# Kernel tuning notes

Measured on AMD Instinct MI355X. Metric: run time of the kernel, lower is better.

## Reference

```python
import jax, jax.numpy as jnp
import numpy as np

N = 100000
E = 1600000
F_IN = 512
S_IN = 6
H = 64
C = 7


def gcn_conv(x, W, b, row, col, n):
    # PyG GCNConv: linear (no bias in lin), add self-loops, sym-normalize, scatter-add, + bias
    x = x @ W  # [N, out]
    loop = jnp.arange(n)
    r = jnp.concatenate([row, loop])
    c = jnp.concatenate([col, loop])
    deg = jax.ops.segment_sum(jnp.ones(r.shape, x.dtype), c, num_segments=n)
    dinv = jnp.where(deg > 0, deg ** -0.5, 0.0)
    norm = dinv[r] * dinv[c]  # [E+N]
    out = jax.ops.segment_sum(x[r] * norm[:, None], c, num_segments=n)
    return out + b


def setup_inputs() -> dict:
    key = jax.random.key(0)
    ks = jax.random.split(key, 12)
    feature = jax.random.normal(ks[0], (N, F_IN), jnp.float32)
    structure = jax.random.normal(ks[1], (N, S_IN), jnp.float32)
    edge_index = jax.random.randint(ks[2], (2, E), 0, N, dtype=jnp.int64)
    # glorot-ish param init
    def w(k, fan_in, fan_out):
        return jax.random.normal(k, (fan_in, fan_out), jnp.float32) * (1.0 / np.sqrt(fan_in))
    return {
        "feature": feature,
        "structure": structure,
        "edge_index": edge_index,
        "W_f": w(ks[3], F_IN, H), "b_f": jnp.zeros((H,), jnp.float32),
        "W_s": w(ks[4], S_IN, H), "b_s": jnp.zeros((H,), jnp.float32),
        "W_r": w(ks[5], 2 * H, C), "b_r": jnp.zeros((C,), jnp.float32),
        "emb": jax.random.normal(ks[6], (6, H), jnp.float32),
        "embW": jax.random.normal(ks[7], (H, 1), jnp.float32),
        "alpha_s": jnp.asarray(0.4, jnp.float32),
        "alpha_a": jnp.asarray(0.6, jnp.float32),
    }


def reference(feature, structure, edge_index, W_f, b_f, W_s, b_s, W_r, b_r, emb, embW, alpha_s, alpha_a):
    row, col = edge_index[0], edge_index[1]
    # branch 1: feature GCN (dropout is identity in eval mode)
    h_f = gcn_conv(feature, W_f, b_f, row, col, N)
    attr = h_f
    # embedding gate: sigmoid(emb @ embW) thresholded at 0.5 -> {0,1}
    gate = jax.nn.sigmoid(emb @ embW)  # [6,1]
    gate = jnp.where(gate < 0.5, 0.0, 1.0).astype(feature.dtype)
    struct_in = structure * gate[:, 0][None, :]  # [N,6] * [1,6]
    # branch 2: structure GCN
    h_s = gcn_conv(struct_in, W_s, b_s, row, col, N)
    struc = h_s
    # L1-normalize alphas (0.4,0.6 already sum to 1; torch does it via .data)
    denom = jax.lax.stop_gradient(jnp.abs(alpha_s) + jnp.abs(alpha_a))
    a_s = alpha_s / denom
    a_a = alpha_a / denom
    x = jnp.concatenate([attr * a_a * 2.0, struc * a_s * 2.0], axis=1)  # [N, 2H]
    y = gcn_conv(x, W_r, b_r, row, col, N)
    return (h_f, h_s, y)
```

## Files before the change

### kernel.cpp

```cpp
#include <hip/hip_runtime.h>
#include <hip/hip_bf16.h>


typedef __attribute__((ext_vector_type(8))) short bf16x8;
typedef __attribute__((ext_vector_type(4))) float f32x4;

__device__ __forceinline__ unsigned short f2bf(float x) {
    union { __hip_bfloat16 b; unsigned short u; } cv;
    cv.b = __float2bfloat16(x);
    return cv.u;
}
__device__ __forceinline__ float bf2f(unsigned short u) {
    union { unsigned u32; float f; } cv;
    cv.u32 = ((unsigned)u) << 16;
    return cv.f;
}

__global__ __launch_bounds__(256) void setup_prep_k(const float* __restrict__ emb,
                                                    const float* __restrict__ embW,
                                                    const float* __restrict__ alpha_s,
                                                    const float* __restrict__ alpha_a,
                                                    float* __restrict__ cw,
                                                    const float* __restrict__ Wf,
                                                    unsigned short* __restrict__ WthG,
                                                    unsigned short* __restrict__ WtlG,
                                                    unsigned* __restrict__ deg, int n) {
    if (blockIdx.x == 0) {
        if (threadIdx.x >= 64) return;
        int lane = threadIdx.x;
        float w = embW[lane];
        #pragma unroll
        for (int k = 0; k < 6; k++) {
            float p = emb[k * 64 + lane] * w;
            #pragma unroll
            for (int off = 32; off; off >>= 1) p += __shfl_xor(p, off);
            if (lane == 0) cw[k] = (p < 0.0f) ? 0.0f : 1.0f;
        }
        if (lane == 0) {
            float s = alpha_s[0];
            float a = alpha_a[0];
            float inv = 1.0f / (fabsf(s) + fabsf(a));
            cw[6] = 2.0f * a * inv;
            cw[7] = 2.0f * s * inv;
        }
        return;
    }
    if (blockIdx.x <= 128) {
        int idx = (blockIdx.x - 1) * 256 + threadIdx.x;
        int k = idx >> 6, c = idx & 63;
        float w = Wf[idx];
        unsigned short h = f2bf(w);
        unsigned short l = f2bf(w - bf2f(h));
        WthG[c * 512 + k] = h;
        WtlG[c * 512 + k] = l;
        return;
    }
    int start = (blockIdx.x - 129) * 1024 + threadIdx.x;
    #pragma unroll
    for (int k = 0; k < 4; k++) {
        int w = start + k * 256;
        if (w < n) deg[w] = 0u;
    }
}

__device__ __forceinline__ bool detect32(const int* p32, int e, int E, int lane) {
    int se = (e < E) ? e : lane;
    return __any(p32[2 * se + 1] != 0);
}

__global__ void degfill_k(const void* __restrict__ ei, unsigned* __restrict__ deg,
                          int* __restrict__ slot, int E) {
    int e = blockIdx.x * 256 + threadIdx.x;
    int lane = threadIdx.x & 63;
    const int* p32 = (const int*)ei;
    bool is32 = detect32(p32, e, E, lane);
    if (e >= E) return;
    int r, c;
    if (is32) {
        r = p32[e]; c = p32[E + e];
    } else {
        const long long* p = (const long long*)ei;
        r = (int)p[e]; c = (int)p[(size_t)E + e];
    }
    unsigned pos = atomicAdd(&deg[c], 1u);
    if (pos < 64u) slot[((size_t)c << 6) + pos] = r;
}

__global__ void dinv_ss6_k(const unsigned* __restrict__ deg, float* __restrict__ dinv,
                           const float* __restrict__ structure, const float* __restrict__ cw,
                           unsigned short* __restrict__ ss6, int n) {
    int i = blockIdx.x * 256 + threadIdx.x;
    if (i >= n) return;
    float dv = rsqrtf((float)deg[i] + 1.0f);
    dinv[i] = dv;
    #pragma unroll
    for (int k = 0; k < 6; k++) ss6[i * 8 + k] = f2bf(structure[i * 6 + k] * cw[k] * dv);
    ss6[i * 8 + 6] = 0;
    ss6[i * 8 + 7] = 0;
}

__global__ __launch_bounds__(256) void gemm_f_mfma(const float* __restrict__ feat,
                                                   const unsigned short* __restrict__ WthG,
                                                   const unsigned short* __restrict__ WtlG,
                                                   const float* __restrict__ dinv,
                                                   unsigned short* __restrict__ xs, int n) {
    __shared__ unsigned short Ah[128 * 64];
    __shared__ unsigned short Bh[64 * 64];
    __shared__ unsigned short Bl[64 * 64];

    const int tid = threadIdx.x;
    const int blk = blockIdx.x;
    const int w = tid >> 6, l = tid & 63;
    const int lr = l & 15, lg = l >> 4;

    f32x4 acc[2][4];
    #pragma unroll
    for (int m = 0; m < 2; m++)
        #pragma unroll
        for (int nt = 0; nt < 4; nt++) acc[m][nt] = (f32x4)(0.0f);

    const int sr = tid >> 1, shalf = tid & 1;
    const int swc = tid >> 2, swq = tid & 3;
    const int gr_ld = min(blk * 128 + sr, n - 1);
    const float* asrc = feat + (size_t)gr_ld * 512 + shalf * 32;

    for (int k0 = 0; k0 < 512; k0 += 64) {
        {
            const float4* s4 = (const float4*)(asrc + k0);
            int base = sr * 128 + shalf * 64;
            int sw = (sr & 7) << 4;
            #pragma unroll
            for (int g = 0; g < 8; g++) {
                float4 v = s4[g];
                ushort4 h;
                h.x = f2bf(v.x); h.y = f2bf(v.y); h.z = f2bf(v.z); h.w = f2bf(v.w);
                *(ushort4*)((char*)Ah + ((base + g * 8) ^ sw)) = h;
            }
        }
        {
            int sw = (swc & 7) << 4;
            const unsigned short* wh = WthG + swc * 512 + k0;
            const unsigned short* wl = WtlG + swc * 512 + k0;
            #pragma unroll
            for (int s = 0; s < 2; s++) {
                int ko16 = swq * 2 + s;
                uint4 vh = *(const uint4*)(wh + ko16 * 8);
                uint4 vl = *(const uint4*)(wl + ko16 * 8);
                int off = (swc * 128 + ko16 * 16) ^ sw;
                *(uint4*)((char*)Bh + off) = vh;
                *(uint4*)((char*)Bl + off) = vl;
            }
        }
        __syncthreads();
        int swl = (lr & 7) << 4;
        #pragma unroll
        for (int ks = 0; ks < 2; ks++) {
            int koff = ks * 64 + lg * 16;
            int ra = ((w * 32 + lr) * 128 + koff) ^ swl;
            bf16x8 ah0 = *(const bf16x8*)((const char*)Ah + ra);
            bf16x8 ah1 = *(const bf16x8*)((const char*)Ah + ra + 16 * 128);
            #pragma unroll
            for (int nt = 0; nt < 4; nt++) {
                int cb = ((nt * 16 + lr) * 128 + koff) ^ swl;
                bf16x8 bh = *(const bf16x8*)((const char*)Bh + cb);
                bf16x8 bl = *(const bf16x8*)((const char*)Bl + cb);
                acc[0][nt] = __builtin_amdgcn_mfma_f32_16x16x32_bf16(ah0, bh, acc[0][nt], 0, 0, 0);
                acc[0][nt] = __builtin_amdgcn_mfma_f32_16x16x32_bf16(ah0, bl, acc[0][nt], 0, 0, 0);
                acc[1][nt] = __builtin_amdgcn_mfma_f32_16x16x32_bf16(ah1, bh, acc[1][nt], 0, 0, 0);
                acc[1][nt] = __builtin_amdgcn_mfma_f32_16x16x32_bf16(ah1, bl, acc[1][nt], 0, 0, 0);
            }
        }
        __syncthreads();
    }
    #pragma unroll
    for (int m = 0; m < 2; m++) {
        int row0 = blk * 128 + w * 32 + m * 16 + lg * 4;
        #pragma unroll
        for (int reg = 0; reg < 4; reg++) {
            int gr = row0 + reg;
            if (gr < n) {
                float dv = dinv[gr];
                #pragma unroll
                for (int nt = 0; nt < 4; nt++)
                    xs[(size_t)gr * 64 + nt * 16 + lr] = f2bf(acc[m][nt][reg] * dv);
            }
        }
    }
}

#define GATHER8(rl, g, accv, a6v)                                              \
    {                                                                          \
        int r0 = __shfl(rl, g + 0), r1 = __shfl(rl, g + 1);                    \
        int r2 = __shfl(rl, g + 2), r3 = __shfl(rl, g + 3);                    \
        int r4 = __shfl(rl, g + 4), r5 = __shfl(rl, g + 5);                    \
        int r6 = __shfl(rl, g + 6), r7 = __shfl(rl, g + 7);                    \
        float v0 = bf2f(xs[(size_t)r0 * 64 + lane]);                           \
        float v1 = bf2f(xs[(size_t)r1 * 64 + lane]);                           \
        float v2 = bf2f(xs[(size_t)r2 * 64 + lane]);                           \
        float v3 = bf2f(xs[(size_t)r3 * 64 + lane]);                           \
        float v4 = bf2f(xs[(size_t)r4 * 64 + lane]);                           \
        float v5 = bf2f(xs[(size_t)r5 * 64 + lane]);                           \
        float v6 = bf2f(xs[(size_t)r6 * 64 + lane]);                           \
        float v7 = bf2f(xs[(size_t)r7 * 64 + lane]);                           \
        accv += ((v0 + v1) + (v2 + v3)) + ((v4 + v5) + (v6 + v7));             \
        if (lane < 6) {                                                        \
            float u0 = bf2f(ss6[r0 * 8 + lane]), u1 = bf2f(ss6[r1 * 8 + lane]);\
            float u2 = bf2f(ss6[r2 * 8 + lane]), u3 = bf2f(ss6[r3 * 8 + lane]);\
            float u4 = bf2f(ss6[r4 * 8 + lane]), u5 = bf2f(ss6[r5 * 8 + lane]);\
            float u6 = bf2f(ss6[r6 * 8 + lane]), u7 = bf2f(ss6[r7 * 8 + lane]);\
            a6v += ((u0 + u1) + (u2 + u3)) + ((u4 + u5) + (u6 + u7));          \
        }                                                                      \
    }

__global__ __launch_bounds__(256) void agg_fs_k(const unsigned short* __restrict__ xs,
                                                const unsigned short* __restrict__ ss6,
                                                const int* __restrict__ slot,
                                                const unsigned* __restrict__ deg,
                                                const float* __restrict__ dinv,
                                                const float* __restrict__ cw,
                                                const float* __restrict__ bfv,
                                                const float* __restrict__ Ws,
                                                const float* __restrict__ bs,
                                                const float* __restrict__ Wr,
                                                float* __restrict__ out_hf,
                                                float* __restrict__ out_hs,
                                                unsigned short* __restrict__ ps, int n) {
    int wid = threadIdx.x >> 6;
    int lane = threadIdx.x & 63;
    int iA = blockIdx.x * 8 + wid * 2;
    int iB = iA + 1;
    if (iA >= n) return;
    bool hasB = iB < n;

    int dA = (int)min(deg[iA], 64u);
    int dB = hasB ? (int)min(deg[iB], 64u) : 0;

    float accA = bf2f(xs[(size_t)iA * 64 + lane]);
    float accB = hasB ? bf2f(xs[(size_t)iB * 64 + lane]) : 0.0f;
    float a6A = (lane < 6) ? bf2f(ss6[iA * 8 + lane]) : 0.0f;
    float a6B = (hasB && lane < 6) ? bf2f(ss6[iB * 8 + lane]) : 0.0f;

    int rlA = (lane < dA) ? slot[((size_t)iA << 6) + lane] : 0;
    int rlB = (lane < dB) ? slot[((size_t)iB << 6) + lane] : 0;
    int gmax = max(dA, dB);
    for (int g = 0; g + 8 <= gmax; g += 8) {
        if (g + 8 <= dA) GATHER8(rlA, g, accA, a6A);
        if (g + 8 <= dB) GATHER8(rlB, g, accB, a6B);
    }
    for (int d = dA & ~7; d < dA; d++) {
        int r = __shfl(rlA, d);
        accA += bf2f(xs[(size_t)r * 64 + lane]);
        if (lane < 6) a6A += bf2f(ss6[r * 8 + lane]);
    }
    for (int d = dB & ~7; d < dB; d++) {
        int r = __shfl(rlB, d);
        accB += bf2f(xs[(size_t)r * 64 + lane]);
        if (lane < 6) a6B += bf2f(ss6[r * 8 + lane]);
    }

    #pragma unroll
    for (int node = 0; node < 2; node++) {
        if (node == 1 && !hasB) break;
        int i = node ? iB : iA;
        float acc = node ? accB : accA;
        float a6 = node ? a6B : a6A;
        float di = dinv[i];
        float hf = acc * di + bfv[lane];
        float hs = bs[lane];
        #pragma unroll
        for (int k = 0; k < 6; k++) hs += __shfl(a6, k) * di * Ws[k * 64 + lane];
        out_hf[(size_t)i * 64 + lane] = hf;
        out_hs[(size_t)i * 64 + lane] = hs;

        float fa = hf * cw[6];
        float sa = hs * cw[7];
        #pragma unroll
        for (int j = 0; j < 7; j++) {
            float v = fa * Wr[lane * 7 + j] + sa * Wr[(64 + lane) * 7 + j];
            #pragma unroll
            for (int off = 32; off; off >>= 1) v += __shfl_xor(v, off);
            if (lane == j) ps[(size_t)i * 8 + j] = f2bf(v * di);
        }
        if (lane == 7) ps[(size_t)i * 8 + 7] = 0;
    }
}

__global__ __launch_bounds__(256) void agg_y_k(const unsigned short* __restrict__ ps,
                                               const int* __restrict__ slot,
                                               const unsigned* __restrict__ deg,
                                               const float* __restrict__ dinv,
                                               const float* __restrict__ br,
                                               float* __restrict__ out_y, int n) {
    int i = blockIdx.x * 4 + (threadIdx.x >> 6);
    int lane = threadIdx.x & 63;
    if (i >= n) return;
    int es = lane >> 3, j = lane & 7;
    int cnt = (int)min(deg[i], 64u);
    const int* srow = slot + ((size_t)i << 6);
    float acc = (es == 0) ? bf2f(ps[(size_t)i * 8 + j]) : 0.0f;
    int base = 0;
    for (; base + 16 <= cnt; base += 16) {
        int ra = srow[base + es];
        int rb = srow[base + 8 + es];
        acc += bf2f(ps[(size_t)ra * 8 + j]) + bf2f(ps[(size_t)rb * 8 + j]);
    }
    for (; base < cnt; base += 8) {
        int idx = base + es;
        if (idx < cnt) acc += bf2f(ps[(size_t)srow[idx] * 8 + j]);
    }
    acc += __shfl_xor(acc, 8);
    acc += __shfl_xor(acc, 16);
    acc += __shfl_xor(acc, 32);
    if (j < 7) out_y[(size_t)i * 7 + j] = acc * dinv[i] + br[j];
}

extern "C" void kernel_launch(void* const* d_in, const int* in_sizes, int n_in,
                              void* d_out, int out_size, void* d_ws, size_t ws_size,
                              hipStream_t stream) {
    const float* feature   = (const float*)d_in[0];
    const float* structure = (const float*)d_in[1];
    const void*  ei        = d_in[2];
    const float* Wf  = (const float*)d_in[3];
    const float* bfv = (const float*)d_in[4];
    const float* Ws  = (const float*)d_in[5];
    const float* bs  = (const float*)d_in[6];
    const float* Wr  = (const float*)d_in[7];
    const float* br  = (const float*)d_in[8];
    const float* emb = (const float*)d_in[9];
    const float* embW = (const float*)d_in[10];
    const float* alpha_s = (const float*)d_in[11];
    const float* alpha_a = (const float*)d_in[12];

    const int N = in_sizes[0] / 512;
    const int E = in_sizes[2] / 2;
    const int NB = (N + 255) / 256;
    const int NZ = (N + 1023) / 1024;

    float* ws = (float*)d_ws;
    size_t XS     = 0;
    size_t SS6    = XS + (size_t)N * 32;
    size_t PS     = SS6 + (size_t)N * 4;
    size_t DINV   = PS + (size_t)N * 4;
    size_t DEG    = DINV + N;
    size_t CW     = DEG + N;
    size_t WT     = CW + 16;
    size_t SLOT   = WT + 32768;

    unsigned short* xs = (unsigned short*)(ws + XS);
    unsigned short* ss6 = (unsigned short*)(ws + SS6);
    unsigned short* ps = (unsigned short*)(ws + PS);
    float* dinv = ws + DINV;
    unsigned* deg = (unsigned*)(ws + DEG);
    float* cw = ws + CW;
    unsigned short* WthG = (unsigned short*)(ws + WT);
    unsigned short* WtlG = WthG + 512 * 64;
    int* slot = (int*)(ws + SLOT);

    setup_prep_k<<<129 + NZ, 256, 0, stream>>>(emb, embW, alpha_s, alpha_a, cw,
                                               Wf, WthG, WtlG, deg, N);
    degfill_k<<<(E + 255) / 256, 256, 0, stream>>>(ei, deg, slot, E);
    dinv_ss6_k<<<NB, 256, 0, stream>>>(deg, dinv, structure, cw, ss6, N);
    gemm_f_mfma<<<(N + 127) / 128, 256, 0, stream>>>(feature, WthG, WtlG, dinv, xs, N);

    float* out_hf = (float*)d_out;
    float* out_hs = out_hf + (size_t)N * 64;
    float* out_y  = out_hf + (size_t)N * 128;
    agg_fs_k<<<(N + 7) / 8, 256, 0, stream>>>(xs, ss6, slot, deg, dinv, cw,
                                              bfv, Ws, bs, Wr, out_hf, out_hs, ps, N);
    agg_y_k<<<(N + 3) / 4, 256, 0, stream>>>(ps, slot, deg, dinv, br, out_y, N);
}
```

Before: 310.7 us.

## Overlap degree/slot fill with feature GEMM in one launch, defer dinv scaling

Edge-degree counting and slot filling now run as the first blocks of a combined kernel alongside the feature GEMM blocks, so the atomic-heavy edge pass can overlap with the memory-bound GEMM. Each edge block now handles 4 edges per thread. Because dinv is not yet known during the GEMM, the GEMM stores unscaled bf16 results, and a new post kernel computes dinv, rescales xs in place and builds ss6. The cost is an extra read-modify-write pass over xs and a second bf16 rounding on it.

```diff
diff --git a/kernel.cpp b/kernel.cpp
--- a/kernel.cpp
+++ b/kernel.cpp
@@ -68,48 +68,50 @@
     return __any(p32[2 * se + 1] != 0);
 }
 
-__global__ void degfill_k(const void* __restrict__ ei, unsigned* __restrict__ deg,
-                          int* __restrict__ slot, int E) {
-    int e = blockIdx.x * 256 + threadIdx.x;
-    int lane = threadIdx.x & 63;
-    const int* p32 = (const int*)ei;
-    bool is32 = detect32(p32, e, E, lane);
-    if (e >= E) return;
-    int r, c;
-    if (is32) {
-        r = p32[e]; c = p32[E + e];
-    } else {
-        const long long* p = (const long long*)ei;
-        r = (int)p[e]; c = (int)p[(size_t)E + e];
-    }
-    unsigned pos = atomicAdd(&deg[c], 1u);
-    if (pos < 64u) slot[((size_t)c << 6) + pos] = r;
-}
-
-__global__ void dinv_ss6_k(const unsigned* __restrict__ deg, float* __restrict__ dinv,
-                           const float* __restrict__ structure, const float* __restrict__ cw,
-                           unsigned short* __restrict__ ss6, int n) {
-    int i = blockIdx.x * 256 + threadIdx.x;
-    if (i >= n) return;
-    float dv = rsqrtf((float)deg[i] + 1.0f);
-    dinv[i] = dv;
-    #pragma unroll
-    for (int k = 0; k < 6; k++) ss6[i * 8 + k] = f2bf(structure[i * 6 + k] * cw[k] * dv);
-    ss6[i * 8 + 6] = 0;
-    ss6[i * 8 + 7] = 0;
-}
-
-__global__ __launch_bounds__(256) void gemm_f_mfma(const float* __restrict__ feat,
-                                                   const unsigned short* __restrict__ WthG,
-                                                   const unsigned short* __restrict__ WtlG,
-                                                   const float* __restrict__ dinv,
-                                                   unsigned short* __restrict__ xs, int n) {
+__global__ __launch_bounds__(256) void fused_k(const void* __restrict__ ei,
+                                               unsigned* __restrict__ deg,
+                                               int* __restrict__ slot, int E, int EB,
+                                               const float* __restrict__ feat,
+                                               const unsigned short* __restrict__ WthG,
+                                               const unsigned short* __restrict__ WtlG,
+                                               unsigned short* __restrict__ xs, int n) {
     __shared__ unsigned short Ah[128 * 64];
     __shared__ unsigned short Bh[64 * 64];
     __shared__ unsigned short Bl[64 * 64];
 
     const int tid = threadIdx.x;
-    const int blk = blockIdx.x;
+    if ((int)blockIdx.x < EB) {
+        int lane = tid & 63;
+        const int* p32 = (const int*)ei;
+        int e0 = blockIdx.x * 1024 + tid;
+        bool is32 = detect32(p32, e0, E, lane);
+        int r[4], c[4];
+        bool v[4];
+        #pragma unroll
+        for (int k = 0; k < 4; k++) {
+            int e = e0 + k * 256;
+            v[k] = e < E;
+            r[k] = 0; c[k] = 0;
+            if (v[k]) {
+                if (is32) {
+                    r[k] = p32[e]; c[k] = p32[E + e];
+                } else {
+                    const long long* p = (const long long*)ei;
+                    r[k] = (int)p[e]; c[k] = (int)p[(size_t)E + e];
+                }
+            }
+        }
+        unsigned pos[4];
+        #pragma unroll
+        for (int k = 0; k < 4; k++)
+            if (v[k]) pos[k] = atomicAdd(&deg[c[k]], 1u);
+        #pragma unroll
+        for (int k = 0; k < 4; k++)
+            if (v[k] && pos[k] < 64u) slot[((size_t)c[k] << 6) + pos[k]] = r[k];
+        return;
+    }
+
+    const int blk = blockIdx.x - EB;
     const int w = tid >> 6, l = tid & 63;
     const int lr = l & 15, lg = l >> 4;
 
@@ -179,13 +181,29 @@
         for (int reg = 0; reg < 4; reg++) {
             int gr = row0 + reg;
             if (gr < n) {
-                float dv = dinv[gr];
                 #pragma unroll
                 for (int nt = 0; nt < 4; nt++)
-                    xs[(size_t)gr * 64 + nt * 16 + lr] = f2bf(acc[m][nt][reg] * dv);
-            }
-        }
-    }
+                    xs[(size_t)gr * 64 + nt * 16 + lr] = f2bf(acc[m][nt][reg]);
+            }
+        }
+    }
+}
+
+__global__ __launch_bounds__(256) void post_k(const unsigned* __restrict__ deg,
+                                              float* __restrict__ dinv,
+                                              const float* __restrict__ structure,
+                                              const float* __restrict__ cw,
+                                              unsigned short* __restrict__ ss6,
+                                              unsigned short* __restrict__ xs, int n) {
+    int i = blockIdx.x * 4 + (threadIdx.x >> 6);
+    int lane = threadIdx.x & 63;
+    if (i >= n) return;
+    float dv = rsqrtf((float)deg[i] + 1.0f);
+    if (lane == 0) dinv[i] = dv;
+    size_t o = (size_t)i * 64 + lane;
+    xs[o] = f2bf(bf2f(xs[o]) * dv);
+    if (lane < 6) ss6[i * 8 + lane] = f2bf(structure[i * 6 + lane] * cw[lane] * dv);
+    if (lane == 6 || lane == 7) ss6[i * 8 + lane] = 0;
 }
 
 #define GATHER8(rl, g, accv, a6v)                                              \
@@ -335,6 +353,8 @@
     const int E = in_sizes[2] / 2;
     const int NB = (N + 255) / 256;
     const int NZ = (N + 1023) / 1024;
+    const int EB = (E + 1023) / 1024;
+    const int GB = (N + 127) / 128;
 
     float* ws = (float*)d_ws;
     size_t XS     = 0;
@@ -358,9 +378,9 @@
 
     setup_prep_k<<<129 + NZ, 256, 0, stream>>>(emb, embW, alpha_s, alpha_a, cw,
                                                Wf, WthG, WtlG, deg, N);
-    degfill_k<<<(E + 255) / 256, 256, 0, stream>>>(ei, deg, slot, E);
-    dinv_ss6_k<<<NB, 256, 0, stream>>>(deg, dinv, structure, cw, ss6, N);
-    gemm_f_mfma<<<(N + 127) / 128, 256, 0, stream>>>(feature, WthG, WtlG, dinv, xs, N);
+    fused_k<<<EB + GB, 256, 0, stream>>>(ei, deg, slot, E, EB,
+                                         feature, WthG, WtlG, xs, N);
+    post_k<<<(N + 3) / 4, 256, 0, stream>>>(deg, dinv, structure, cw, ss6, xs, N);
 
     float* out_hf = (float*)d_out;
     float* out_hs = out_hf + (size_t)N * 64;
```

New measurement: 326.2 us. 1.05x slower.

## Partition degree/slot fill by destination range across blocks

Applied to the files above, without the earlier changes.

Each edge chunk of 4096 is now processed by 8 blocks, each of which handles only edges whose destination falls in one eighth of the node range. Blocks working at the same time therefore aim their atomics and slot writes at a narrower region of deg and slot, which is meant to improve L2 locality and spread atomic traffic across XCDs/channels. The cost is that the column indices are read 8 times, and each thread takes more branches.

```diff
diff --git a/kernel.cpp b/kernel.cpp
--- a/kernel.cpp
+++ b/kernel.cpp
@@ -68,22 +68,36 @@
     return __any(p32[2 * se + 1] != 0);
 }
 
-__global__ void degfill_k(const void* __restrict__ ei, unsigned* __restrict__ deg,
-                          int* __restrict__ slot, int E) {
-    int e = blockIdx.x * 256 + threadIdx.x;
+#define CHUNK 4096
+__global__ __launch_bounds__(256) void degfill_k(const void* __restrict__ ei,
+                                                 unsigned* __restrict__ deg,
+                                                 int* __restrict__ slot, int E, int n) {
+    int range = blockIdx.x & 7;
+    int nper = (n + 7) >> 3;
+    int lo = range * nper;
+    int hi = min(n, lo + nper);
+    int e0 = (blockIdx.x >> 3) * CHUNK + threadIdx.x;
     int lane = threadIdx.x & 63;
     const int* p32 = (const int*)ei;
-    bool is32 = detect32(p32, e, E, lane);
-    if (e >= E) return;
-    int r, c;
-    if (is32) {
-        r = p32[e]; c = p32[E + e];
-    } else {
-        const long long* p = (const long long*)ei;
-        r = (int)p[e]; c = (int)p[(size_t)E + e];
-    }
-    unsigned pos = atomicAdd(&deg[c], 1u);
-    if (pos < 64u) slot[((size_t)c << 6) + pos] = r;
+    bool is32 = detect32(p32, e0, E, lane);
+
+    int cs[16];
+    #pragma unroll
+    for (int k = 0; k < 16; k++) {
+        int e = e0 + k * 256;
+        cs[k] = -1;
+        if (e < E)
+            cs[k] = is32 ? p32[E + e] : (int)((const long long*)ei)[(size_t)E + e];
+    }
+    #pragma unroll
+    for (int k = 0; k < 16; k++) {
+        int c = cs[k];
+        if (c < lo || c >= hi) continue;
+        int e = e0 + k * 256;
+        int r = is32 ? p32[e] : (int)((const long long*)ei)[(size_t)e];
+        unsigned pos = atomicAdd(&deg[c], 1u);
+        if (pos < 64u) slot[((size_t)c << 6) + pos] = r;
+    }
 }
 
 __global__ void dinv_ss6_k(const unsigned* __restrict__ deg, float* __restrict__ dinv,
@@ -335,6 +349,7 @@
     const int E = in_sizes[2] / 2;
     const int NB = (N + 255) / 256;
     const int NZ = (N + 1023) / 1024;
+    const int NCH = (E + CHUNK - 1) / CHUNK;
 
     float* ws = (float*)d_ws;
     size_t XS     = 0;
@@ -358,7 +373,7 @@
 
     setup_prep_k<<<129 + NZ, 256, 0, stream>>>(emb, embW, alpha_s, alpha_a, cw,
                                                Wf, WthG, WtlG, deg, N);
-    degfill_k<<<(E + 255) / 256, 256, 0, stream>>>(ei, deg, slot, E);
+    degfill_k<<<NCH * 8, 256, 0, stream>>>(ei, deg, slot, E, N);
     dinv_ss6_k<<<NB, 256, 0, stream>>>(deg, dinv, structure, cw, ss6, N);
     gemm_f_mfma<<<(N + 127) / 128, 256, 0, stream>>>(feature, WthG, WtlG, dinv, xs, N);
 
```

Result: faster. 281.8 us (-9.3%).
